# Kernel tuning notes

Measured on AMD Instinct MI355X. Metric: run time of the kernel, lower is better.

Reference implementation:

```python
import jax, jax.numpy as jnp
import numpy as np

NUM_GROUPS = 8   # conv groups and GroupNorm groups (get_safe_groups(256,8)==8)
EPS = 1e-5


def setup_inputs() -> dict:
    key = jax.random.key(0)
    k_x, k_w, k_rw, k_ri, k_g, k_b = jax.random.split(key, 6)
    B, Cin, H, W = 8, 256, 64, 64
    E, Cout, K = 8, 256, 2
    x = jax.random.normal(k_x, (B, Cin, H, W), jnp.float32)
    # grouped conv weight: (E*Cout, Cin//groups, 3, 3)
    conv_w = jax.random.normal(k_w, (E * Cout, Cin // NUM_GROUPS, 3, 3), jnp.float32) * 0.02
    routing_weights = jax.random.uniform(k_rw, (B, K), jnp.float32)
    routing_indices = jax.random.randint(k_ri, (B, K), 0, E)
    gamma = 1.0 + 0.1 * jax.random.normal(k_g, (E, Cout), jnp.float32)
    beta = 0.1 * jax.random.normal(k_b, (E, Cout), jnp.float32)
    return {"x": x, "routing_weights": routing_weights, "routing_indices": routing_indices,
            "top_k": K, "conv_w": conv_w, "gamma": gamma, "beta": beta}


def reference(x, routing_weights, routing_indices, top_k, conv_w, gamma, beta):
    B, Cin, H, W = x.shape
    E, Cout = gamma.shape
    # fused grouped 3x3 conv, padding=1, no bias
    fused = jax.lax.conv_general_dilated(
        x, conv_w, window_strides=(1, 1), padding=((1, 1), (1, 1)),
        dimension_numbers=("NCHW", "OIHW", "NCHW"), feature_group_count=NUM_GROUPS)
    fused = fused.reshape(B, E, Cout, H, W)
    idx = routing_indices.reshape(B, top_k)
    wts = routing_weights.reshape(B, top_k)
    # gather the top_k expert outputs per sample: [B, K, Cout, H, W]
    sel = jnp.take_along_axis(fused, idx[:, :, None, None, None], axis=1)
    # per-expert GroupNorm in fp32 with gamma/beta gathered by expert id
    G = NUM_GROUPS
    xs = sel.astype(jnp.float32).reshape(B, top_k, G, Cout // G, H, W)
    mu = xs.mean(axis=(3, 4, 5), keepdims=True)
    var = xs.var(axis=(3, 4, 5), keepdims=True)
    normed = ((xs - mu) * jax.lax.rsqrt(var + EPS)).reshape(B, top_k, Cout, H, W)
    g = gamma[idx][:, :, :, None, None]   # [B, K, Cout, 1, 1]
    b = beta[idx][:, :, :, None, None]
    normed = (normed * g + b).astype(sel.dtype)
    # SiLU then weighted combine over top_k
    act = normed * jax.nn.sigmoid(normed)
    out = jnp.sum(act * wts[:, :, None, None, None], axis=1)  # [B, Cout, H, W]
    return out
```

## Files before the change

kernel.cpp:

```cpp
#include <hip/hip_runtime.h>

typedef __attribute__((ext_vector_type(8))) short bf8_t;
typedef __attribute__((ext_vector_type(4))) float f4_t;

#define BATCH 8
#define HW    4096
#define COUT  256
#define KTOP  2
#define NPAIR 16
#define NG    8
#define EPSV  1e-5f
#define XSTR  40

#define OFF_CONV  0
#define OFF_XTP   8388608
#define OFF_WTB   (8388608 + 1393920)
#define OFF_STATS (8388608 + 1393920 + 294912)

__device__ __forceinline__ unsigned short f2bf(float f) {
    unsigned u = __builtin_bit_cast(unsigned, f);
    u = (u + 0x7FFFu + ((u >> 16) & 1u)) >> 16;
    return (unsigned short)u;
}
__device__ __forceinline__ float bf2f(unsigned short h) {
    return __builtin_bit_cast(float, (unsigned)h << 16);
}

__global__ void prep_w(const float* __restrict__ w, unsigned short* __restrict__ wTb,
                       float* __restrict__ stats) {
    __shared__ float ls[32 * 288];
    const int tid = threadIdx.x;
    const int e   = blockIdx.x >> 3;
    const int cb  = (blockIdx.x & 7) * 32;
    if (blockIdx.x == 0 && tid < NPAIR * NG * 2) stats[tid] = 0.f;
    const float4* src = (const float4*)(w + (size_t)(e * 256 + cb) * 288);
    for (int f = tid; f < 2304; f += 256) ((float4*)ls)[f] = src[f];
    __syncthreads();
    for (int idx = tid; idx < 9216; idx += 256) {
        int tap = idx >> 10;
        int rem = idx & 1023;
        int cc  = rem >> 5;
        int i   = rem & 31;
        wTb[((size_t)(e * 9 + tap) * 256 + cb + cc) * 32 + i] = f2bf(ls[cc * 288 + i * 9 + tap]);
    }
}

__global__ void prep_x(const float* __restrict__ x, const int* __restrict__ ridx,
                       unsigned short* __restrict__ xtp) {
    __shared__ float t[32][65];
    const int r   = blockIdx.x;
    const int p   = blockIdx.y;
    const int b   = p >> 1;
    const int e   = ridx[p];
    const int tid = threadIdx.x;
    const bool inter = (r >= 1 && r <= 64);
    if (inter) {
        const float* xb = x + (((size_t)b * 256 + e * 32) * 64 + (r - 1)) * 64;
        for (int f = tid; f < 2048; f += 256)
            t[f >> 6][f & 63] = xb[(size_t)(f >> 6) * 4096 + (f & 63)];
    }
    __syncthreads();
    unsigned short* ob = xtp + ((size_t)p * 66 + r) * (66 * XSTR);
    for (int f = tid; f < 1056; f += 256) {
        int c = f >> 4, chp = f & 15;
        ushort2 v = make_ushort2(0, 0);
        if (inter && c >= 1 && c <= 64)
            v = make_ushort2(f2bf(t[2 * chp][c - 1]), f2bf(t[2 * chp + 1][c - 1]));
        *(ushort2*)(ob + c * XSTR + chp * 2) = v;
    }
}

__launch_bounds__(512, 4)
__global__ void conv_mfma(const unsigned short* __restrict__ xtp,
                          const unsigned short* __restrict__ wTb,
                          const int* __restrict__ ridx,
                          unsigned short* __restrict__ convbuf,
                          float* __restrict__ stats)
{
    __shared__ short xs[4 * 66 * XSTR];

    const int tid = threadIdx.x;
    const int st  = blockIdx.x;
    const int p   = blockIdx.y;
    const int e   = ridx[p];

    {
        const unsigned short* g = xtp + ((size_t)p * 66 + st * 2) * (66 * XSTR);
        for (int f = tid; f < 1320; f += 512)
            *(bf8_t*)&xs[f * 8] = *(const bf8_t*)(g + f * 8);
    }
    __syncthreads();

    const int lane = tid & 63;
    const int l15  = lane & 15;
    const int oct  = lane >> 4;
    const int wave = tid >> 6;
    const int wc   = wave & 3;
    const int ws   = wave >> 2;

    const short* Ab = xs + (ws * 66 + l15) * XSTR + oct * 8;
    const unsigned short* Bb = wTb + ((size_t)e * 9 * 256 + wc * 64 + l15) * 32 + oct * 8;

    f4_t acc[4][4];
    #pragma unroll
    for (int mi = 0; mi < 4; ++mi)
        #pragma unroll
        for (int ni = 0; ni < 4; ++ni)
            acc[mi][ni] = (f4_t){0.f, 0.f, 0.f, 0.f};

    bf8_t bw[2][4];
    #pragma unroll
    for (int ni = 0; ni < 4; ++ni)
        bw[0][ni] = *(const bf8_t*)(Bb + ni * 512);

    #pragma unroll
    for (int tap = 0; tap < 9; ++tap) {
        const int dy = tap / 3, dx = tap % 3;
        if (tap < 8) {
            #pragma unroll
            for (int ni = 0; ni < 4; ++ni)
                bw[(tap + 1) & 1][ni] = *(const bf8_t*)(Bb + (tap + 1) * 8192 + ni * 512);
        }
        bf8_t ax[4];
        #pragma unroll
        for (int mi = 0; mi < 4; ++mi)
            ax[mi] = *(const bf8_t*)(Ab + (dy * 66 + mi * 16 + dx) * XSTR);
        #pragma unroll
        for (int mi = 0; mi < 4; ++mi)
            #pragma unroll
            for (int ni = 0; ni < 4; ++ni)
                acc[mi][ni] = __builtin_amdgcn_mfma_f32_16x16x32_bf16(
                    ax[mi], bw[tap & 1][ni], acc[mi][ni], 0, 0, 0);
    }

    const int sp0 = st * 128 + ws * 64 + oct * 4;
    float s0 = 0.f, q0 = 0.f, s1 = 0.f, q1 = 0.f;
    #pragma unroll
    for (int ni = 0; ni < 4; ++ni) {
        const size_t crow = ((size_t)p * 256 + wc * 64 + ni * 16 + l15) * 4096;
        #pragma unroll
        for (int mi = 0; mi < 4; ++mi) {
            float a0 = acc[mi][ni][0], a1 = acc[mi][ni][1];
            float a2 = acc[mi][ni][2], a3 = acc[mi][ni][3];
            ushort4 pk = make_ushort4(f2bf(a0), f2bf(a1), f2bf(a2), f2bf(a3));
            *(ushort4*)(convbuf + crow + sp0 + mi * 16) = pk;
            float sl = a0 + a1 + a2 + a3;
            float ql = fmaf(a0, a0, fmaf(a1, a1, fmaf(a2, a2, a3 * a3)));
            if (ni < 2) { s0 += sl; q0 += ql; }
            else        { s1 += sl; q1 += ql; }
        }
    }
    #pragma unroll
    for (int m = 32; m >= 1; m >>= 1) {
        s0 += __shfl_xor(s0, m); q0 += __shfl_xor(q0, m);
        s1 += __shfl_xor(s1, m); q1 += __shfl_xor(q1, m);
    }
    if (lane == 0) {
        int g0 = wc * 2;
        atomicAdd(&stats[(p * 8 + g0) * 2 + 0], s0);
        atomicAdd(&stats[(p * 8 + g0) * 2 + 1], q0);
        atomicAdd(&stats[(p * 8 + g0 + 1) * 2 + 0], s1);
        atomicAdd(&stats[(p * 8 + g0 + 1) * 2 + 1], q1);
    }
}

__global__ void finalize_k(const unsigned short* __restrict__ conv,
                           const float* __restrict__ stats,
                           const int* __restrict__ ridx,
                           const float* __restrict__ rw,
                           const float* __restrict__ gamma,
                           const float* __restrict__ beta,
                           float* __restrict__ out)
{
    const int tid = threadIdx.x;
    const int c   = blockIdx.x;
    const int b   = blockIdx.y;
    const int g   = c >> 5;

    float ga[2], be[2], wk[2];
    const unsigned short* cb[2];
    #pragma unroll
    for (int k = 0; k < KTOP; ++k) {
        int p = b * KTOP + k;
        int e = ridx[p];
        wk[k] = rw[p];
        float s  = stats[(p * 8 + g) * 2 + 0];
        float sq = stats[(p * 8 + g) * 2 + 1];
        const float cnt = 1.f / 131072.f;
        float mu  = s * cnt;
        float var = fmaf(-mu, mu, sq * cnt);
        float inv = rsqrtf(var + EPSV);
        ga[k] = gamma[e * 256 + c] * inv;
        be[k] = fmaf(-mu, ga[k], beta[e * 256 + c]);
        cb[k] = conv + ((size_t)p * 256 + c) * 4096;
    }
    float* ob = out + ((size_t)b * 256 + c) * 4096;
    #pragma unroll
    for (int j = 0; j < 4; ++j) {
        int sp = j * 1024 + tid * 4;
        float r0 = 0.f, r1 = 0.f, r2 = 0.f, r3 = 0.f;
        #pragma unroll
        for (int k = 0; k < KTOP; ++k) {
            ushort4 v = *(const ushort4*)(cb[k] + sp);
            float n0 = fmaf(bf2f(v.x), ga[k], be[k]);
            float n1 = fmaf(bf2f(v.y), ga[k], be[k]);
            float n2 = fmaf(bf2f(v.z), ga[k], be[k]);
            float n3 = fmaf(bf2f(v.w), ga[k], be[k]);
            r0 = fmaf(wk[k] * n0, 1.f / (1.f + __expf(-n0)), r0);
            r1 = fmaf(wk[k] * n1, 1.f / (1.f + __expf(-n1)), r1);
            r2 = fmaf(wk[k] * n2, 1.f / (1.f + __expf(-n2)), r2);
            r3 = fmaf(wk[k] * n3, 1.f / (1.f + __expf(-n3)), r3);
        }
        *(float4*)(ob + sp) = make_float4(r0, r1, r2, r3);
    }
}

extern "C" void kernel_launch(void* const* d_in, const int* in_sizes, int n_in,
                              void* d_out, int out_size, void* d_ws, size_t ws_size,
                              hipStream_t stream) {
    const float* x      = (const float*)d_in[0];
    const float* rw     = (const float*)d_in[1];
    const int*   ridx   = (const int*)  d_in[2];
    const float* conv_w = (const float*)d_in[4];
    const float* gamma  = (const float*)d_in[5];
    const float* beta   = (const float*)d_in[6];
    float* out = (float*)d_out;

    float* ws = (float*)d_ws;
    unsigned short* convbuf = (unsigned short*)(ws + OFF_CONV);
    unsigned short* xtp     = (unsigned short*)(ws + OFF_XTP);
    unsigned short* wTb     = (unsigned short*)(ws + OFF_WTB);
    float*          stats   = ws + OFF_STATS;

    hipLaunchKernelGGL(prep_w, dim3(64), dim3(256), 0, stream, conv_w, wTb, stats);
    hipLaunchKernelGGL(prep_x, dim3(66, 16), dim3(256), 0, stream, x, ridx, xtp);
    hipLaunchKernelGGL(conv_mfma, dim3(32, 16), dim3(512), 0, stream,
                       xtp, wTb, ridx, convbuf, stats);
    hipLaunchKernelGGL(finalize_k, dim3(256, 8), dim3(256), 0, stream,
                       convbuf, stats, ridx, rw, gamma, beta, out);
}
```

Before: 162.5 us.

## Recompute conv in apply pass instead of storing bf16 intermediate; merge prep kernels

The conv output is no longer written to a bf16 buffer. A stats-only conv pass accumulates the GroupNorm sums, then a second conv pass recomputes both expert convolutions per sample and applies normalization, SiLU and the weighted combine directly from the accumulators, writing fp32 output. The two prep kernels are merged into one launch and the weight double-buffer prefetch is dropped. This trades a 16 MB intermediate write and read for doubling the MFMA work. It also changes the output store pattern to strided 16-element scalar writes and uses a lower occupancy bound.

```diff
diff --git a/kernel.cpp b/kernel.cpp
--- a/kernel.cpp
+++ b/kernel.cpp
@@ -3,79 +3,72 @@
 typedef __attribute__((ext_vector_type(8))) short bf8_t;
 typedef __attribute__((ext_vector_type(4))) float f4_t;
 
-#define BATCH 8
-#define HW    4096
-#define COUT  256
 #define KTOP  2
 #define NPAIR 16
 #define NG    8
 #define EPSV  1e-5f
 #define XSTR  40
 
-#define OFF_CONV  0
-#define OFF_XTP   8388608
-#define OFF_WTB   (8388608 + 1393920)
-#define OFF_STATS (8388608 + 1393920 + 294912)
+#define OFF_XTP   0
+#define OFF_WTB   1393920
+#define OFF_STATS (1393920 + 294912)
 
 __device__ __forceinline__ unsigned short f2bf(float f) {
     unsigned u = __builtin_bit_cast(unsigned, f);
     u = (u + 0x7FFFu + ((u >> 16) & 1u)) >> 16;
     return (unsigned short)u;
 }
-__device__ __forceinline__ float bf2f(unsigned short h) {
-    return __builtin_bit_cast(float, (unsigned)h << 16);
-}
-
-__global__ void prep_w(const float* __restrict__ w, unsigned short* __restrict__ wTb,
-                       float* __restrict__ stats) {
-    __shared__ float ls[32 * 288];
+
+__global__ void prep(const float* __restrict__ w, const float* __restrict__ x,
+                     const int* __restrict__ ridx,
+                     unsigned short* __restrict__ wTb,
+                     unsigned short* __restrict__ xtp,
+                     float* __restrict__ stats)
+{
+    __shared__ float sh[32 * 288];
     const int tid = threadIdx.x;
-    const int e   = blockIdx.x >> 3;
-    const int cb  = (blockIdx.x & 7) * 32;
-    if (blockIdx.x == 0 && tid < NPAIR * NG * 2) stats[tid] = 0.f;
-    const float4* src = (const float4*)(w + (size_t)(e * 256 + cb) * 288);
-    for (int f = tid; f < 2304; f += 256) ((float4*)ls)[f] = src[f];
-    __syncthreads();
-    for (int idx = tid; idx < 9216; idx += 256) {
-        int tap = idx >> 10;
-        int rem = idx & 1023;
-        int cc  = rem >> 5;
-        int i   = rem & 31;
-        wTb[((size_t)(e * 9 + tap) * 256 + cb + cc) * 32 + i] = f2bf(ls[cc * 288 + i * 9 + tap]);
-    }
-}
-
-__global__ void prep_x(const float* __restrict__ x, const int* __restrict__ ridx,
-                       unsigned short* __restrict__ xtp) {
-    __shared__ float t[32][65];
-    const int r   = blockIdx.x;
-    const int p   = blockIdx.y;
-    const int b   = p >> 1;
-    const int e   = ridx[p];
-    const int tid = threadIdx.x;
-    const bool inter = (r >= 1 && r <= 64);
-    if (inter) {
-        const float* xb = x + (((size_t)b * 256 + e * 32) * 64 + (r - 1)) * 64;
-        for (int f = tid; f < 2048; f += 256)
-            t[f >> 6][f & 63] = xb[(size_t)(f >> 6) * 4096 + (f & 63)];
-    }
-    __syncthreads();
-    unsigned short* ob = xtp + ((size_t)p * 66 + r) * (66 * XSTR);
-    for (int f = tid; f < 1056; f += 256) {
-        int c = f >> 4, chp = f & 15;
-        ushort2 v = make_ushort2(0, 0);
-        if (inter && c >= 1 && c <= 64)
-            v = make_ushort2(f2bf(t[2 * chp][c - 1]), f2bf(t[2 * chp + 1][c - 1]));
-        *(ushort2*)(ob + c * XSTR + chp * 2) = v;
+    if (blockIdx.x < 64) {
+        const int e  = blockIdx.x >> 3;
+        const int cb = (blockIdx.x & 7) * 32;
+        if (blockIdx.x == 0 && tid < NPAIR * NG * 2) stats[tid] = 0.f;
+        const float4* src = (const float4*)(w + (size_t)(e * 256 + cb) * 288);
+        for (int f = tid; f < 2304; f += 256) ((float4*)sh)[f] = src[f];
+        __syncthreads();
+        for (int idx = tid; idx < 9216; idx += 256) {
+            int tap = idx >> 10, rem = idx & 1023, cc = rem >> 5, i = rem & 31;
+            wTb[((size_t)(e * 9 + tap) * 256 + cb + cc) * 32 + i] =
+                f2bf(sh[cc * 288 + i * 9 + tap]);
+        }
+    } else {
+        float (*t)[65] = (float(*)[65])sh;
+        const int idx = blockIdx.x - 64;
+        const int p   = idx / 66;
+        const int r   = idx - p * 66;
+        const int b   = p >> 1;
+        const int e   = ridx[p];
+        const bool inter = (r >= 1 && r <= 64);
+        if (inter) {
+            const float* xb = x + (((size_t)b * 256 + e * 32) * 64 + (r - 1)) * 64;
+            for (int f = tid; f < 2048; f += 256)
+                t[f >> 6][f & 63] = xb[(size_t)(f >> 6) * 4096 + (f & 63)];
+        }
+        __syncthreads();
+        unsigned short* ob = xtp + ((size_t)p * 66 + r) * (66 * XSTR);
+        for (int f = tid; f < 1056; f += 256) {
+            int c = f >> 4, chp = f & 15;
+            ushort2 v = make_ushort2(0, 0);
+            if (inter && c >= 1 && c <= 64)
+                v = make_ushort2(f2bf(t[2 * chp][c - 1]), f2bf(t[2 * chp + 1][c - 1]));
+            *(ushort2*)(ob + c * XSTR + chp * 2) = v;
+        }
     }
 }
 
 __launch_bounds__(512, 4)
-__global__ void conv_mfma(const unsigned short* __restrict__ xtp,
-                          const unsigned short* __restrict__ wTb,
-                          const int* __restrict__ ridx,
-                          unsigned short* __restrict__ convbuf,
-                          float* __restrict__ stats)
+__global__ void conv_stats(const unsigned short* __restrict__ xtp,
+                           const unsigned short* __restrict__ wTb,
+                           const int* __restrict__ ridx,
+                           float* __restrict__ stats)
 {
     __shared__ short xs[4 * 66 * XSTR];
 
@@ -91,14 +84,10 @@
     }
     __syncthreads();
 
-    const int lane = tid & 63;
-    const int l15  = lane & 15;
-    const int oct  = lane >> 4;
-    const int wave = tid >> 6;
-    const int wc   = wave & 3;
-    const int ws   = wave >> 2;
-
-    const short* Ab = xs + (ws * 66 + l15) * XSTR + oct * 8;
+    const int lane = tid & 63, l15 = lane & 15, oct = lane >> 4;
+    const int wave = tid >> 6, wc = wave & 3, wsp = wave >> 2;
+
+    const short* Ab = xs + (wsp * 66 + l15) * XSTR + oct * 8;
     const unsigned short* Bb = wTb + ((size_t)e * 9 * 256 + wc * 64 + l15) * 32 + oct * 8;
 
     f4_t acc[4][4];
@@ -107,49 +96,36 @@
         #pragma unroll
         for (int ni = 0; ni < 4; ++ni)
             acc[mi][ni] = (f4_t){0.f, 0.f, 0.f, 0.f};
-
-    bf8_t bw[2][4];
-    #pragma unroll
-    for (int ni = 0; ni < 4; ++ni)
-        bw[0][ni] = *(const bf8_t*)(Bb + ni * 512);
 
     #pragma unroll
     for (int tap = 0; tap < 9; ++tap) {
         const int dy = tap / 3, dx = tap % 3;
-        if (tap < 8) {
-            #pragma unroll
-            for (int ni = 0; ni < 4; ++ni)
-                bw[(tap + 1) & 1][ni] = *(const bf8_t*)(Bb + (tap + 1) * 8192 + ni * 512);
-        }
-        bf8_t ax[4];
+        bf8_t ax[4], bw[4];
         #pragma unroll
         for (int mi = 0; mi < 4; ++mi)
             ax[mi] = *(const bf8_t*)(Ab + (dy * 66 + mi * 16 + dx) * XSTR);
         #pragma unroll
+        for (int ni = 0; ni < 4; ++ni)
+            bw[ni] = *(const bf8_t*)(Bb + tap * 8192 + ni * 512);
+        #pragma unroll
         for (int mi = 0; mi < 4; ++mi)
             #pragma unroll
             for (int ni = 0; ni < 4; ++ni)
                 acc[mi][ni] = __builtin_amdgcn_mfma_f32_16x16x32_bf16(
-                    ax[mi], bw[tap & 1][ni], acc[mi][ni], 0, 0, 0);
-    }
-
-    const int sp0 = st * 128 + ws * 64 + oct * 4;
+                    ax[mi], bw[ni], acc[mi][ni], 0, 0, 0);
+    }
+
     float s0 = 0.f, q0 = 0.f, s1 = 0.f, q1 = 0.f;
     #pragma unroll
-    for (int ni = 0; ni < 4; ++ni) {
-        const size_t crow = ((size_t)p * 256 + wc * 64 + ni * 16 + l15) * 4096;
-        #pragma unroll
-        for (int mi = 0; mi < 4; ++mi) {
-            float a0 = acc[mi][ni][0], a1 = acc[mi][ni][1];
-            float a2 = acc[mi][ni][2], a3 = acc[mi][ni][3];
-            ushort4 pk = make_ushort4(f2bf(a0), f2bf(a1), f2bf(a2), f2bf(a3));
-            *(ushort4*)(convbuf + crow + sp0 + mi * 16) = pk;
-            float sl = a0 + a1 + a2 + a3;
-            float ql = fmaf(a0, a0, fmaf(a1, a1, fmaf(a2, a2, a3 * a3)));
-            if (ni < 2) { s0 += sl; q0 += ql; }
-            else        { s1 += sl; q1 += ql; }
-        }
-    }
+    for (int mi = 0; mi < 4; ++mi)
+        #pragma unroll
+        for (int ni = 0; ni < 4; ++ni)
+            #pragma unroll
+            for (int r = 0; r < 4; ++r) {
+                float v = acc[mi][ni][r];
+                if (ni < 2) { s0 += v; q0 = fmaf(v, v, q0); }
+                else        { s1 += v; q1 = fmaf(v, v, q1); }
+            }
     #pragma unroll
     for (int m = 32; m >= 1; m >>= 1) {
         s0 += __shfl_xor(s0, m); q0 += __shfl_xor(q0, m);
@@ -164,55 +140,119 @@
     }
 }
 
-__global__ void finalize_k(const unsigned short* __restrict__ conv,
-                           const float* __restrict__ stats,
+__launch_bounds__(512, 2)
+__global__ void conv_apply(const unsigned short* __restrict__ xtp,
+                           const unsigned short* __restrict__ wTb,
                            const int* __restrict__ ridx,
                            const float* __restrict__ rw,
                            const float* __restrict__ gamma,
                            const float* __restrict__ beta,
+                           const float* __restrict__ stats,
                            float* __restrict__ out)
 {
+    __shared__ short  xs[2][4 * 66 * XSTR];
+    __shared__ float2 gab[2][256];
+
     const int tid = threadIdx.x;
-    const int c   = blockIdx.x;
+    const int st  = blockIdx.x;
     const int b   = blockIdx.y;
-    const int g   = c >> 5;
-
-    float ga[2], be[2], wk[2];
-    const unsigned short* cb[2];
-    #pragma unroll
-    for (int k = 0; k < KTOP; ++k) {
+
+    {
+        int k = tid >> 8, c = tid & 255;
         int p = b * KTOP + k;
         int e = ridx[p];
-        wk[k] = rw[p];
+        int g = c >> 5;
         float s  = stats[(p * 8 + g) * 2 + 0];
-        float sq = stats[(p * 8 + g) * 2 + 1];
+        float q  = stats[(p * 8 + g) * 2 + 1];
         const float cnt = 1.f / 131072.f;
         float mu  = s * cnt;
-        float var = fmaf(-mu, mu, sq * cnt);
+        float var = fmaf(-mu, mu, q * cnt);
         float inv = rsqrtf(var + EPSV);
-        ga[k] = gamma[e * 256 + c] * inv;
-        be[k] = fmaf(-mu, ga[k], beta[e * 256 + c]);
-        cb[k] = conv + ((size_t)p * 256 + c) * 4096;
-    }
-    float* ob = out + ((size_t)b * 256 + c) * 4096;
-    #pragma unroll
-    for (int j = 0; j < 4; ++j) {
-        int sp = j * 1024 + tid * 4;
-        float r0 = 0.f, r1 = 0.f, r2 = 0.f, r3 = 0.f;
-        #pragma unroll
-        for (int k = 0; k < KTOP; ++k) {
-            ushort4 v = *(const ushort4*)(cb[k] + sp);
-            float n0 = fmaf(bf2f(v.x), ga[k], be[k]);
-            float n1 = fmaf(bf2f(v.y), ga[k], be[k]);
-            float n2 = fmaf(bf2f(v.z), ga[k], be[k]);
-            float n3 = fmaf(bf2f(v.w), ga[k], be[k]);
-            r0 = fmaf(wk[k] * n0, 1.f / (1.f + __expf(-n0)), r0);
-            r1 = fmaf(wk[k] * n1, 1.f / (1.f + __expf(-n1)), r1);
-            r2 = fmaf(wk[k] * n2, 1.f / (1.f + __expf(-n2)), r2);
-            r3 = fmaf(wk[k] * n3, 1.f / (1.f + __expf(-n3)), r3);
-        }
-        *(float4*)(ob + sp) = make_float4(r0, r1, r2, r3);
-    }
+        float ga  = gamma[e * 256 + c] * inv;
+        float be  = fmaf(-mu, ga, beta[e * 256 + c]);
+        gab[k][c] = make_float2(ga, be);
+    }
+    {
+        const unsigned short* g0 = xtp + ((size_t)(b * KTOP + 0) * 66 + st * 2) * (66 * XSTR);
+        const unsigned short* g1 = xtp + ((size_t)(b * KTOP + 1) * 66 + st * 2) * (66 * XSTR);
+        for (int f = tid; f < 2640; f += 512) {
+            const unsigned short* s = (f < 1320) ? (g0 + f * 8) : (g1 + (f - 1320) * 8);
+            *(bf8_t*)&xs[0][f * 8] = *(const bf8_t*)s;
+        }
+    }
+    __syncthreads();
+
+    const int lane = tid & 63, l15 = lane & 15, oct = lane >> 4;
+    const int wave = tid >> 6, wc = wave & 3, wsp = wave >> 2;
+
+    f4_t res[4][4];
+    #pragma unroll
+    for (int mi = 0; mi < 4; ++mi)
+        #pragma unroll
+        for (int ni = 0; ni < 4; ++ni)
+            res[mi][ni] = (f4_t){0.f, 0.f, 0.f, 0.f};
+
+    #pragma unroll
+    for (int k = 0; k < KTOP; ++k) {
+        const int p = b * KTOP + k;
+        const int e = ridx[p];
+        const unsigned short* Ab = wTb + ((size_t)e * 9 * 256 + wc * 64 + l15) * 32 + oct * 8;
+        const short* Bb = &xs[k][0] + (wsp * 66 + l15) * XSTR + oct * 8;
+
+        f4_t acc[4][4];
+        #pragma unroll
+        for (int mi = 0; mi < 4; ++mi)
+            #pragma unroll
+            for (int ni = 0; ni < 4; ++ni)
+                acc[mi][ni] = (f4_t){0.f, 0.f, 0.f, 0.f};
+
+        #pragma unroll
+        for (int tap = 0; tap < 9; ++tap) {
+            const int dy = tap / 3, dx = tap % 3;
+            bf8_t aw[4], bx[4];
+            #pragma unroll
+            for (int mi = 0; mi < 4; ++mi)
+                aw[mi] = *(const bf8_t*)(Ab + tap * 8192 + mi * 512);
+            #pragma unroll
+            for (int ni = 0; ni < 4; ++ni)
+                bx[ni] = *(const bf8_t*)(Bb + (dy * 66 + ni * 16 + dx) * XSTR);
+            #pragma unroll
+            for (int mi = 0; mi < 4; ++mi)
+                #pragma unroll
+                for (int ni = 0; ni < 4; ++ni)
+                    acc[mi][ni] = __builtin_amdgcn_mfma_f32_16x16x32_bf16(
+                        aw[mi], bx[ni], acc[mi][ni], 0, 0, 0);
+        }
+
+        const float wk = rw[p];
+        #pragma unroll
+        for (int mi = 0; mi < 4; ++mi) {
+            float2 gb[4];
+            #pragma unroll
+            for (int r = 0; r < 4; ++r)
+                gb[r] = gab[k][wc * 64 + mi * 16 + oct * 4 + r];
+            #pragma unroll
+            for (int ni = 0; ni < 4; ++ni)
+                #pragma unroll
+                for (int r = 0; r < 4; ++r) {
+                    float n  = fmaf(acc[mi][ni][r], gb[r].x, gb[r].y);
+                    float sg = __builtin_amdgcn_rcpf(1.f + __expf(-n));
+                    res[mi][ni][r] = fmaf(wk * n, sg, res[mi][ni][r]);
+                }
+        }
+    }
+
+    const int row = st * 2 + wsp;
+    #pragma unroll
+    for (int mi = 0; mi < 4; ++mi)
+        #pragma unroll
+        for (int r = 0; r < 4; ++r) {
+            float* ob = out + ((size_t)(b * 256 + wc * 64 + mi * 16 + oct * 4 + r)) * 4096
+                            + row * 64 + l15;
+            #pragma unroll
+            for (int ni = 0; ni < 4; ++ni)
+                ob[ni * 16] = res[mi][ni][r];
+        }
 }
 
 extern "C" void kernel_launch(void* const* d_in, const int* in_sizes, int n_in,
@@ -227,15 +267,14 @@
     float* out = (float*)d_out;
 
     float* ws = (float*)d_ws;
-    unsigned short* convbuf = (unsigned short*)(ws + OFF_CONV);
-    unsigned short* xtp     = (unsigned short*)(ws + OFF_XTP);
-    unsigned short* wTb     = (unsigned short*)(ws + OFF_WTB);
-    float*          stats   = ws + OFF_STATS;
-
-    hipLaunchKernelGGL(prep_w, dim3(64), dim3(256), 0, stream, conv_w, wTb, stats);
-    hipLaunchKernelGGL(prep_x, dim3(66, 16), dim3(256), 0, stream, x, ridx, xtp);
-    hipLaunchKernelGGL(conv_mfma, dim3(32, 16), dim3(512), 0, stream,
-                       xtp, wTb, ridx, convbuf, stats);
-    hipLaunchKernelGGL(finalize_k, dim3(256, 8), dim3(256), 0, stream,
-                       convbuf, stats, ridx, rw, gamma, beta, out);
-}
+    unsigned short* xtp   = (unsigned short*)(ws + OFF_XTP);
+    unsigned short* wTb   = (unsigned short*)(ws + OFF_WTB);
+    float*          stats = ws + OFF_STATS;
+
+    hipLaunchKernelGGL(prep, dim3(64 + 16 * 66), dim3(256), 0, stream,
+                       conv_w, x, ridx, wTb, xtp, stats);
+    hipLaunchKernelGGL(conv_stats, dim3(32, 16), dim3(512), 0, stream,
+                       xtp, wTb, ridx, stats);
+    hipLaunchKernelGGL(conv_apply, dim3(32, 8), dim3(512), 0, stream,
+                       xtp, wTb, ridx, rw, gamma, beta, stats, out);
+}
```

New measurement: 150.6 us. 1.08x faster.
